# Kernel tuning notes

Measured on AMD Instinct MI355X. Metric: run time of the kernel, lower is better.

## Reference

```python
import jax, jax.numpy as jnp
import numpy as np

N, E, D, G = 20000, 640000, 256, 64
BN_EPS = 1e-5


def setup_inputs() -> dict:
    key = jax.random.key(0)
    ks = jax.random.split(key, 16)
    p = lambda k, sh: jax.random.normal(k, sh, dtype=jnp.float32) * 0.05
    x = jax.random.normal(ks[0], (N, D), dtype=jnp.float32)
    edge_index = jax.random.randint(ks[1], (2, E), 0, N, dtype=jnp.int32)
    batch = jnp.sort(jax.random.randint(ks[2], (N,), 0, G, dtype=jnp.int32))
    return dict(
        x=x, edge_index=edge_index, batch=batch,
        W1=p(ks[3], (D, D)), a1_src=p(ks[4], (D,)), a1_dst=p(ks[5], (D,)), b1=p(ks[6], (D,)),
        W2=p(ks[7], (D, D)), a2_src=p(ks[8], (D,)), a2_dst=p(ks[9], (D,)), b2=p(ks[10], (D,)),
        bn_gamma=jnp.ones((D,), jnp.float32), bn_beta=jnp.zeros((D,), jnp.float32),
        bn_mean=jnp.zeros((D,), jnp.float32), bn_var=jnp.ones((D,), jnp.float32),
        Wl=p(ks[11], (D, D)), bl=p(ks[12], (D,)),
    )


def gat_conv(x, src, dst, W, a_src, a_dst, b):
    # PyG GATConv, heads=1, concat=True, negative_slope=0.2, self-loops already appended
    h = x @ W                               # [N, D]
    alpha_s = h @ a_src                     # [N]
    alpha_d = h @ a_dst                     # [N]
    e = jax.nn.leaky_relu(alpha_s[src] + alpha_d[dst], 0.2)   # [E+N]
    # segment softmax over edges grouped by destination node
    m = jax.ops.segment_max(e, dst, num_segments=N)
    ex = jnp.exp(e - m[dst])
    s = jax.ops.segment_sum(ex, dst, num_segments=N)
    alpha = ex / s[dst]                     # self-loops guarantee s > 0
    out = jax.ops.segment_sum(alpha[:, None] * h[src], dst, num_segments=N)
    return out + b


def reference(x, edge_index, batch, W1, a1_src, a1_dst, b1, W2, a2_src, a2_dst, b2,
              bn_gamma, bn_beta, bn_mean, bn_var, Wl, bl):
    loop = jnp.arange(N, dtype=edge_index.dtype)
    src = jnp.concatenate([edge_index[0], loop])
    dst = jnp.concatenate([edge_index[1], loop])

    h = jax.nn.leaky_relu(gat_conv(x, src, dst, W1, a1_src, a1_dst, b1), 0.01)
    h = jax.nn.leaky_relu(gat_conv(h, src, dst, W2, a2_src, a2_dst, b2), 0.01)
    # BatchNorm over nodes (eval mode, running stats)
    h = (h - bn_mean) * jax.lax.rsqrt(bn_var + BN_EPS) * bn_gamma + bn_beta
    # global mean pool per graph, then linear (dropout is identity in eval)
    sums = jax.ops.segment_sum(h, batch, num_segments=G)           # [G, D]
    cnt = jax.ops.segment_sum(jnp.ones((N,), h.dtype), batch, num_segments=G)
    pooled = sums / jnp.maximum(cnt, 1.0)[:, None]
    return pooled @ Wl.T + bl
```

## Files before the change

kernel.cpp:

```cpp
#include <hip/hip_runtime.h>
#include <hip/hip_bf16.h>

#define NN 20000
#define EE 640000
#define DD 256
#define GG 64
#define ETOT (EE + NN)
#define BN_EPS 1e-5f

#define NPART 8
#define PBLK  128
#define CE    (EE / PBLK)
#define PRNG  (NN / NPART)

#define GBM 64
#define GBN 128
#define GBK 64
#define NGEMMB 626
#define SCE 1023

typedef short s16x8 __attribute__((ext_vector_type(8)));
typedef float f32x4 __attribute__((ext_vector_type(4)));
typedef int   i32x2 __attribute__((ext_vector_type(2)));
typedef int   i32x4 __attribute__((ext_vector_type(4)));

__device__ __forceinline__ unsigned short f2bf_hi(float x) {
    unsigned u = __float_as_uint(x);
    unsigned r = (u + 0x7FFFu + ((u >> 16) & 1u)) >> 16;
    return (unsigned short)r;
}
__device__ __forceinline__ float bf2f(unsigned short h) {
    return __uint_as_float(((unsigned)h) << 16);
}

__device__ __forceinline__ void fma8(const short* __restrict__ hb, int row, int f0,
                                     float a, float* acc) {
    i32x4 hv = *(const i32x4*)(hb + (size_t)row * DD + f0);
    #pragma unroll
    for (int k = 0; k < 4; ++k) {
        unsigned u = (unsigned)hv[k];
        acc[2 * k]     += a * __uint_as_float(u << 16);
        acc[2 * k + 1] += a * __uint_as_float(u & 0xFFFF0000u);
    }
}

__global__ __launch_bounds__(256) void prep_hist_conv_kernel(
        const int* __restrict__ batch, int* __restrict__ start, float* __restrict__ cntf,
        const int* __restrict__ ei, int* __restrict__ counts,
        const float* __restrict__ W1, const float* __restrict__ W2,
        short* __restrict__ BhT1, short* __restrict__ BlT1,
        short* __restrict__ BhT2, short* __restrict__ BlT2) {
    int b = blockIdx.x;
    int r = b & 15, G = b >> 4;
    if (r < 8) {
        int lo = (b & 7) * PRNG;
        int e0 = G * CE;
        for (int i = e0 + threadIdx.x; i < e0 + CE; i += 256) {
            int d = ei[EE + i];
            if ((unsigned)(d - lo) < (unsigned)PRNG) atomicAdd(&counts[d], 1);
        }
        return;
    }
    int idx = G * 8 + (r - 8);
    if (idx < 512) {
        int n = idx & 255, which = idx >> 8;
        int k = threadIdx.x;
        const float* B = which ? W2 : W1;
        short* Bh = which ? BhT2 : BhT1;
        short* Bl = which ? BlT2 : BlT1;
        float x = B[k * DD + n];
        unsigned short hbv = f2bf_hi(x);
        Bh[n * DD + k] = (short)hbv;
        Bl[n * DD + k] = (short)f2bf_hi(x - bf2f(hbv));
    } else if (idx == 512) {
        int g = threadIdx.x;
        if (g <= GG) {
            if (g == GG) start[GG] = NN;
            else {
                int lo = 0, hi = NN;
                while (lo < hi) { int mid = (lo + hi) >> 1; if (batch[mid] < g) lo = mid + 1; else hi = mid; }
                start[g] = lo;
            }
        }
        __syncthreads();
        if (g < GG) cntf[g] = (float)(start[g + 1] - start[g]);
    }
}

#define SCHUNK 20
__global__ __launch_bounds__(1024) void scan_kernel(const int* __restrict__ counts,
                                                    int* __restrict__ offsets,
                                                    int* __restrict__ cursor) {
    __shared__ int wsums[16];
    int t = threadIdx.x, lane = t & 63, wid = t >> 6;
    int base = t * SCHUNK;
    int loc[SCHUNK];
    int sum = 0;
    #pragma unroll
    for (int i = 0; i < SCHUNK; ++i) {
        int idx = base + i;
        int v = (idx < NN) ? (counts[idx] + 1) : 0;
        loc[i] = sum; sum += v;
    }
    int x = sum;
    #pragma unroll
    for (int o = 1; o < 64; o <<= 1) { int tv = __shfl_up(x, o, 64); if (lane >= o) x += tv; }
    if (lane == 63) wsums[wid] = x;
    __syncthreads();
    if (wid == 0) {
        int wv = (lane < 16) ? wsums[lane] : 0;
        #pragma unroll
        for (int o = 1; o < 16; o <<= 1) { int tv = __shfl_up(wv, o, 64); if (lane >= o) wv += tv; }
        if (lane < 16) wsums[lane] = wv;
    }
    __syncthreads();
    int tbase = (wid ? wsums[wid - 1] : 0) + x - sum;
    #pragma unroll
    for (int i = 0; i < SCHUNK; ++i) {
        int idx = base + i;
        if (idx < NN) { int e = tbase + loc[i]; offsets[idx] = e; cursor[idx] = e; }
    }
    if (t == 0) offsets[NN] = wsums[15];
}

template<bool SCAT>
__global__ __launch_bounds__(256) void gemm_kernel(
        const float* __restrict__ A,
        const short* __restrict__ BhT, const short* __restrict__ BlT,
        const float* __restrict__ a_src, const float* __restrict__ a_dst,
        short* __restrict__ hb, float* __restrict__ asp, float* __restrict__ adp, int M,
        const int* __restrict__ ei, int* __restrict__ cursor, int* __restrict__ csr_src) {
    __shared__ short As_h[GBM * GBK];
    __shared__ short As_l[GBM * GBK];
    __shared__ short Bs_h[GBN * GBK];
    __shared__ short Bs_l[GBN * GBK];
    int tid = threadIdx.x;
    int gx = blockIdx.x, gy = blockIdx.y;
    int row0 = gy * GBM;
    int col0 = gx * GBN;
    int w = tid >> 6, lane = tid & 63;
    int wr = w >> 1, wc = w & 1;

    f32x4 acc[2][4];
    #pragma unroll
    for (int m = 0; m < 2; ++m)
        #pragma unroll
        for (int n = 0; n < 4; ++n)
            acc[m][n] = (f32x4){0.f, 0.f, 0.f, 0.f};

    int srow = tid >> 3;
    int sslot = tid & 7;

    for (int k0 = 0; k0 < DD; k0 += GBK) {
        __syncthreads();
        #pragma unroll
        for (int p = 0; p < 2; ++p) {
            int r = p * 32 + srow;
            int gr = row0 + r;
            float xv[8];
            if (gr < M) {
                const float4* ap = (const float4*)(A + (size_t)gr * DD + k0 + sslot * 8);
                float4 a0 = ap[0], a1 = ap[1];
                xv[0] = a0.x; xv[1] = a0.y; xv[2] = a0.z; xv[3] = a0.w;
                xv[4] = a1.x; xv[5] = a1.y; xv[6] = a1.z; xv[7] = a1.w;
            } else {
                #pragma unroll
                for (int i = 0; i < 8; ++i) xv[i] = 0.f;
            }
            s16x8 hv, lv;
            #pragma unroll
            for (int i = 0; i < 8; ++i) {
                unsigned short hbb = f2bf_hi(xv[i]);
                hv[i] = (short)hbb;
                lv[i] = (short)f2bf_hi(xv[i] - bf2f(hbb));
            }
            int byte = r * 128 + ((sslot ^ (r & 7)) << 4);
            *(s16x8*)((char*)As_h + byte) = hv;
            *(s16x8*)((char*)As_l + byte) = lv;
        }
        #pragma unroll
        for (int p = 0; p < 4; ++p) {
            int r = p * 32 + srow;
            int byte = r * 128 + ((sslot ^ (r & 7)) << 4);
            const short* bhp = BhT + (size_t)(col0 + r) * DD + k0 + sslot * 8;
            const short* blp = BlT + (size_t)(col0 + r) * DD + k0 + sslot * 8;
            *(s16x8*)((char*)Bs_h + byte) = *(const s16x8*)bhp;
            *(s16x8*)((char*)Bs_l + byte) = *(const s16x8*)blp;
        }
        __syncthreads();

        #pragma unroll
        for (int ks = 0; ks < 2; ++ks) {
            s16x8 ah[2], al[2], bh[4], bl[4];
            int g = ks * 4 + (lane >> 4);
            #pragma unroll
            for (int m = 0; m < 2; ++m) {
                int r = wr * 32 + m * 16 + (lane & 15);
                int byte = r * 128 + ((g ^ (r & 7)) << 4);
                ah[m] = *(const s16x8*)((char*)As_h + byte);
                al[m] = *(const s16x8*)((char*)As_l + byte);
            }
            #pragma unroll
            for (int n = 0; n < 4; ++n) {
                int c = wc * 64 + n * 16 + (lane & 15);
                int byte = c * 128 + ((g ^ (c & 7)) << 4);
                bh[n] = *(const s16x8*)((char*)Bs_h + byte);
                bl[n] = *(const s16x8*)((char*)Bs_l + byte);
            }
            #pragma unroll
            for (int m = 0; m < 2; ++m)
                #pragma unroll
                for (int n = 0; n < 4; ++n) {
                    acc[m][n] = __builtin_amdgcn_mfma_f32_16x16x32_bf16(ah[m], bh[n], acc[m][n], 0, 0, 0);
                    acc[m][n] = __builtin_amdgcn_mfma_f32_16x16x32_bf16(ah[m], bl[n], acc[m][n], 0, 0, 0);
                    acc[m][n] = __builtin_amdgcn_mfma_f32_16x16x32_bf16(al[m], bh[n], acc[m][n], 0, 0, 0);
                }
        }
    }

    float vsrc[4], vdst[4];
    #pragma unroll
    for (int n = 0; n < 4; ++n) {
        int cg = col0 + wc * 64 + n * 16 + (lane & 15);
        vsrc[n] = a_src[cg];
        vdst[n] = a_dst[cg];
    }
    #pragma unroll
    for (int m = 0; m < 2; ++m) {
        #pragma unroll
        for (int j = 0; j < 4; ++j) {
            float ps = 0.f, pd = 0.f;
            #pragma unroll
            for (int n = 0; n < 4; ++n) {
                float c = acc[m][n][j];
                ps += c * vsrc[n];
                pd += c * vdst[n];
            }
            #pragma unroll
            for (int o = 1; o < 16; o <<= 1) {
                ps += __shfl_xor(ps, o, 64);
                pd += __shfl_xor(pd, o, 64);
            }
            if ((lane & 15) == 0) {
                int rg = row0 + wr * 32 + m * 16 + ((lane >> 4) << 2) + j;
                if (rg < M) {
                    asp[(size_t)(gx * 2 + wc) * NN + rg] = ps;
                    adp[(size_t)(gx * 2 + wc) * NN + rg] = pd;
                }
            }
        }
    }

    #pragma unroll
    for (int m = 0; m < 2; ++m) {
        int rbase = row0 + wr * 32 + m * 16 + ((lane >> 4) << 2);
        #pragma unroll
        for (int n = 0; n < 4; ++n) {
            int cg = col0 + wc * 64 + n * 16 + (lane & 15);
            #pragma unroll
            for (int j = 0; j < 4; ++j) {
                int rg = rbase + j;
                if (rg < M) hb[(size_t)rg * DD + cg] = (short)f2bf_hi(acc[m][n][j]);
            }
        }
    }

    if (SCAT) {
        int bid = gy * 2 + gx;
        int e0 = bid * SCE;
        int e1 = min(e0 + SCE, EE);
        for (int i = e0 + tid; i < e1; i += 256) {
            int d = ei[EE + i];
            int pos = atomicAdd(&cursor[d], 1);
            csr_src[pos] = ei[i];
        }
    }
}

__global__ void reduce_kernel(const float* __restrict__ asp, const float* __restrict__ adp,
                              const int* __restrict__ offsets,
                              float* __restrict__ as_, float* __restrict__ ad_,
                              int* __restrict__ csr_src) {
    int i = blockIdx.x * blockDim.x + threadIdx.x;
    if (i < NN) {
        as_[i] = asp[i] + asp[NN + i] + asp[2 * NN + i] + asp[3 * NN + i];
        ad_[i] = adp[i] + adp[NN + i] + adp[2 * NN + i] + adp[3 * NN + i];
        csr_src[offsets[i + 1] - 1] = i;
    }
}

__global__ __launch_bounds__(256) void alpha_kernel(const int* __restrict__ csr_src,
                                                    const int* __restrict__ offsets,
                                                    const float* __restrict__ as_,
                                                    const float* __restrict__ ad_,
                                                    int2* __restrict__ pairs) {
    int tid = threadIdx.x;
    int w = tid >> 6, lane = tid & 63;
    int node = blockIdx.x * 4 + w;
    int off = offsets[node];
    int deg = offsets[node + 1] - off;
    float adn = ad_[node];

    if (deg <= 64) {
        int si = 0; float e = -INFINITY;
        if (lane < deg) {
            si = csr_src[off + lane];
            float t = as_[si] + adn;
            e = (t > 0.f) ? t : 0.2f * t;
        }
        float m = e;
        #pragma unroll
        for (int o = 32; o > 0; o >>= 1) m = fmaxf(m, __shfl_xor(m, o, 64));
        float ex = (lane < deg) ? expf(e - m) : 0.f;
        float s = ex;
        #pragma unroll
        for (int o = 32; o > 0; o >>= 1) s += __shfl_xor(s, o, 64);
        if (lane < deg) {
            int2 p; p.x = si; p.y = __float_as_int(ex / s);
            pairs[off + lane] = p;
        }
        return;
    }

    float m = -INFINITY, s = 0.f;
    for (int cs = 0; cs < deg; cs += 64) {
        int cl = min(64, deg - cs);
        float e = -INFINITY;
        if (lane < cl) {
            int si = csr_src[off + cs + lane];
            float t = as_[si] + adn;
            e = (t > 0.f) ? t : 0.2f * t;
        }
        float cm = e;
        #pragma unroll
        for (int o = 32; o > 0; o >>= 1) cm = fmaxf(cm, __shfl_xor(cm, o, 64));
        float newm = fmaxf(m, cm);
        float ex = (lane < cl) ? expf(e - newm) : 0.f;
        float csum = ex;
        #pragma unroll
        for (int o = 32; o > 0; o >>= 1) csum += __shfl_xor(csum, o, 64);
        s = s * expf(m - newm) + csum;
        m = newm;
    }
    float inv = 1.f / s;
    for (int cs = 0; cs < deg; cs += 64) {
        int cl = min(64, deg - cs);
        if (lane < cl) {
            int si = csr_src[off + cs + lane];
            float t = as_[si] + adn;
            float e = (t > 0.f) ? t : 0.2f * t;
            int2 p; p.x = si; p.y = __float_as_int(expf(e - m) * inv);
            pairs[off + cs + lane] = p;
        }
    }
}

__global__ __launch_bounds__(256) void aggregate_kernel(const short* __restrict__ hb,
                                                        const int2* __restrict__ pairs,
                                                        const int* __restrict__ offsets,
                                                        const float* __restrict__ bias,
                                                        float* __restrict__ out) {
    int tid = threadIdx.x;
    int w = tid >> 6, lane = tid & 63;
    int b = blockIdx.x;
    int sl = b & 3;
    int node = ((b >> 2) << 2) + w;
    int eg = lane >> 3;
    int fl = lane & 7;
    int f0 = sl * 64 + fl * 8;
    int off = offsets[node];
    int deg = offsets[node + 1] - off;
    const i32x2* pp = (const i32x2*)pairs + off;

    float accA[8], accB[8];
    #pragma unroll
    for (int k = 0; k < 8; ++k) { accA[k] = 0.f; accB[k] = 0.f; }

    int j = 0;
    i32x2 qA, qB;
    if (deg >= 16) { qA = pp[eg]; qB = pp[8 + eg]; }
    for (; j + 32 <= deg; j += 16) {
        i32x2 nA = pp[j + 16 + eg];
        i32x2 nB = pp[j + 24 + eg];
        fma8(hb, qA.x, f0, __int_as_float(qA.y), accA);
        fma8(hb, qB.x, f0, __int_as_float(qB.y), accB);
        qA = nA; qB = nB;
    }
    if (j + 16 <= deg) {
        fma8(hb, qA.x, f0, __int_as_float(qA.y), accA);
        fma8(hb, qB.x, f0, __int_as_float(qB.y), accB);
        j += 16;
    }
    {
        if (j + eg < deg) {
            i32x2 p = pp[j + eg];
            fma8(hb, p.x, f0, __int_as_float(p.y), accA);
        }
        if (j + 8 + eg < deg) {
            i32x2 p = pp[j + 8 + eg];
            fma8(hb, p.x, f0, __int_as_float(p.y), accB);
        }
    }

    f32x4 r0, r1;
    #pragma unroll
    for (int k = 0; k < 8; ++k) {
        float v = accA[k] + accB[k];
        v += __shfl_xor(v, 8, 64);
        v += __shfl_xor(v, 16, 64);
        v += __shfl_xor(v, 32, 64);
        if (k < 4) r0[k] = v; else r1[k - 4] = v;
    }
    if (eg == 0) {
        const f32x4 b0 = *(const f32x4*)(bias + f0);
        const f32x4 b1 = *(const f32x4*)(bias + f0 + 4);
        #pragma unroll
        for (int k = 0; k < 4; ++k) {
            float v0 = r0[k] + b0[k];
            float v1 = r1[k] + b1[k];
            r0[k] = (v0 > 0.f) ? v0 : 0.01f * v0;
            r1[k] = (v1 > 0.f) ? v1 : 0.01f * v1;
        }
        __builtin_nontemporal_store(r0, (f32x4*)(out + (size_t)node * DD + f0));
        __builtin_nontemporal_store(r1, (f32x4*)(out + (size_t)node * DD + f0 + 4));
    }
}

#define PSLICE 8
__global__ __launch_bounds__(256) void pool_kernel(const float* __restrict__ h,
                                                   const int* __restrict__ start,
                                                   float* __restrict__ pool) {
    int g = blockIdx.x >> 3, sl = blockIdx.x & (PSLICE - 1);
    int f = threadIdx.x;
    int s0 = start[g], s1 = start[g + 1];
    float acc = 0.f;
    for (int nd = s0 + sl; nd < s1; nd += PSLICE)
        acc += h[(size_t)nd * DD + f];
    if (acc != 0.f || sl == 0) atomicAdd(&pool[g * DD + f], acc);
}

__global__ __launch_bounds__(256) void final_kernel(const float* __restrict__ pool,
                                                    const float* __restrict__ cnt,
                                                    const float* __restrict__ gam,
                                                    const float* __restrict__ bet,
                                                    const float* __restrict__ mean,
                                                    const float* __restrict__ var,
                                                    const float* __restrict__ Wl,
                                                    const float* __restrict__ bl,
                                                    float* __restrict__ out) {
    __shared__ float p_sh[DD];
    int g = blockIdx.x, j = threadIdx.x;
    float cn = cnt[g];
    float scale = gam[j] * rsqrtf(var[j] + BN_EPS);
    p_sh[j] = (cn > 0.f) ? (pool[g * DD + j] / cn - mean[j]) * scale + bet[j] : 0.f;
    __syncthreads();
    float acc = 0.f;
    for (int fi = 0; fi < DD; ++fi)
        acc += p_sh[fi] * Wl[j * DD + fi];
    out[g * DD + j] = acc + bl[j];
}

extern "C" void kernel_launch(void* const* d_in, const int* in_sizes, int n_in,
                              void* d_out, int out_size, void* d_ws, size_t ws_size,
                              hipStream_t stream) {
    const float* x       = (const float*)d_in[0];
    const int*   ei      = (const int*)d_in[1];
    const int*   batch   = (const int*)d_in[2];
    const float* W1      = (const float*)d_in[3];
    const float* a1_src  = (const float*)d_in[4];
    const float* a1_dst  = (const float*)d_in[5];
    const float* b1      = (const float*)d_in[6];
    const float* W2      = (const float*)d_in[7];
    const float* a2_src  = (const float*)d_in[8];
    const float* a2_dst  = (const float*)d_in[9];
    const float* b2      = (const float*)d_in[10];
    const float* bn_g    = (const float*)d_in[11];
    const float* bn_b    = (const float*)d_in[12];
    const float* bn_m    = (const float*)d_in[13];
    const float* bn_v    = (const float*)d_in[14];
    const float* Wl      = (const float*)d_in[15];
    const float* bl      = (const float*)d_in[16];
    float* out = (float*)d_out;

    char* ws = (char*)d_ws;
    size_t o = 0;
    auto take = [&](size_t bytes) { char* p = ws + o; o += (bytes + 255) & ~(size_t)255; return p; };
    int*   counts  = (int*)  take(NN * 4);
    int*   offsets = (int*)  take((NN + 1) * 4);
    int*   cursor  = (int*)  take(NN * 4);
    int*   csr_src = (int*)  take((size_t)ETOT * 4);
    int2*  pairs   = (int2*) take((size_t)ETOT * 8);
    float* asp     = (float*)take((size_t)4 * NN * 4);
    float* adp     = (float*)take((size_t)4 * NN * 4);
    float* as_     = (float*)take(NN * 4);
    float* ad_     = (float*)take(NN * 4);
    short* hb      = (short*)take((size_t)NN * DD * 2);
    float* bufB    = (float*)take((size_t)NN * DD * 4);
    float* pool    = (float*)take(GG * DD * 4);
    float* cnt     = (float*)take(GG * 4);
    int*   start   = (int*)  take((GG + 1) * 4);
    short* BhT1    = (short*)take((size_t)DD * DD * 2);
    short* BlT1    = (short*)take((size_t)DD * DD * 2);
    short* BhT2    = (short*)take((size_t)DD * DD * 2);
    short* BlT2    = (short*)take((size_t)DD * DD * 2);
    (void)ws_size; (void)in_sizes; (void)n_in; (void)out_size;

    hipMemsetAsync(counts, 0, NN * 4, stream);
    hipMemsetAsync(pool, 0, GG * DD * 4, stream);

    prep_hist_conv_kernel<<<2048, 256, 0, stream>>>(batch, start, cnt, ei, counts,
                                                    W1, W2, BhT1, BlT1, BhT2, BlT2);
    scan_kernel<<<1, 1024, 0, stream>>>(counts, offsets, cursor);

    dim3 ggrid(DD / GBN, (NN + GBM - 1) / GBM);

    gemm_kernel<true><<<ggrid, 256, 0, stream>>>(x, BhT1, BlT1, a1_src, a1_dst,
                                                 hb, asp, adp, NN, ei, cursor, csr_src);
    reduce_kernel<<<(NN + 255) / 256, 256, 0, stream>>>(asp, adp, offsets, as_, ad_, csr_src);
    alpha_kernel<<<NN / 4, 256, 0, stream>>>(csr_src, offsets, as_, ad_, pairs);
    aggregate_kernel<<<NN, 256, 0, stream>>>(hb, pairs, offsets, b1, bufB);

    gemm_kernel<false><<<ggrid, 256, 0, stream>>>(bufB, BhT2, BlT2, a2_src, a2_dst,
                                                  hb, asp, adp, NN, nullptr, nullptr, nullptr);
    reduce_kernel<<<(NN + 255) / 256, 256, 0, stream>>>(asp, adp, offsets, as_, ad_, csr_src);
    alpha_kernel<<<NN / 4, 256, 0, stream>>>(csr_src, offsets, as_, ad_, pairs);
    aggregate_kernel<<<NN, 256, 0, stream>>>(hb, pairs, offsets, b2, bufB);

    pool_kernel<<<GG * PSLICE, 256, 0, stream>>>(bufB, start, pool);
    final_kernel<<<GG, 256, 0, stream>>>(pool, cnt, bn_g, bn_b, bn_m, bn_v, Wl, bl, out);
}
```

Baseline: 275.0 us.

## Partition CSR scatter by destination range and pre-shift source indices to byte offsets

The CSR fill inside the first GEMM now has each block scan a larger edge chunk and keep only edges whose destination falls in one of 8 node ranges. Atomics and csr_src writes from a block therefore land in a narrower, more L2-local region, at the cost of each edge index being read 8 times. Separately, the alpha kernel stores source indices pre-multiplied by the row byte stride (si<<9). This lets the aggregate kernel address hb rows with a plain byte offset instead of a 64-bit multiply per gather. The GEMM grid is also flattened to 1D.

```diff
diff --git a/kernel.cpp b/kernel.cpp
--- a/kernel.cpp
+++ b/kernel.cpp
@@ -17,7 +17,8 @@
 #define GBN 128
 #define GBK 64
 #define NGEMMB 626
-#define SCE 1023
+#define SCHUNKS 78
+#define SCSZ 8206
 
 typedef short s16x8 __attribute__((ext_vector_type(8)));
 typedef float f32x4 __attribute__((ext_vector_type(4)));
@@ -33,9 +34,9 @@
     return __uint_as_float(((unsigned)h) << 16);
 }
 
-__device__ __forceinline__ void fma8(const short* __restrict__ hb, int row, int f0,
-                                     float a, float* acc) {
-    i32x4 hv = *(const i32x4*)(hb + (size_t)row * DD + f0);
+__device__ __forceinline__ void fma8o(const char* __restrict__ hbF, int boff,
+                                      float a, float* acc) {
+    i32x4 hv = *(const i32x4*)(hbF + boff);
     #pragma unroll
     for (int k = 0; k < 4; ++k) {
         unsigned u = (unsigned)hv[k];
@@ -135,7 +136,8 @@
     __shared__ short Bs_h[GBN * GBK];
     __shared__ short Bs_l[GBN * GBK];
     int tid = threadIdx.x;
-    int gx = blockIdx.x, gy = blockIdx.y;
+    int lid = blockIdx.x;
+    int gx = lid & 1, gy = lid >> 1;
     int row0 = gy * GBM;
     int col0 = gx * GBN;
     int w = tid >> 6, lane = tid & 63;
@@ -265,14 +267,17 @@
         }
     }
 
-    if (SCAT) {
-        int bid = gy * 2 + gx;
-        int e0 = bid * SCE;
-        int e1 = min(e0 + SCE, EE);
+    if (SCAT && lid < SCHUNKS * NPART) {
+        int part = lid & 7;
+        int lo = part * PRNG;
+        int e0 = (lid >> 3) * SCSZ;
+        int e1 = min(e0 + SCSZ, EE);
         for (int i = e0 + tid; i < e1; i += 256) {
             int d = ei[EE + i];
-            int pos = atomicAdd(&cursor[d], 1);
-            csr_src[pos] = ei[i];
+            if ((unsigned)(d - lo) < (unsigned)PRNG) {
+                int pos = atomicAdd(&cursor[d], 1);
+                csr_src[pos] = ei[i];
+            }
         }
     }
 }
@@ -316,7 +321,7 @@
         #pragma unroll
         for (int o = 32; o > 0; o >>= 1) s += __shfl_xor(s, o, 64);
         if (lane < deg) {
-            int2 p; p.x = si; p.y = __float_as_int(ex / s);
+            int2 p; p.x = si << 9; p.y = __float_as_int(ex / s);
             pairs[off + lane] = p;
         }
         return;
@@ -349,7 +354,7 @@
             int si = csr_src[off + cs + lane];
             float t = as_[si] + adn;
             float e = (t > 0.f) ? t : 0.2f * t;
-            int2 p; p.x = si; p.y = __float_as_int(expf(e - m) * inv);
+            int2 p; p.x = si << 9; p.y = __float_as_int(expf(e - m) * inv);
             pairs[off + cs + lane] = p;
         }
     }
@@ -368,6 +373,7 @@
     int eg = lane >> 3;
     int fl = lane & 7;
     int f0 = sl * 64 + fl * 8;
+    const char* hbF = (const char*)hb + f0 * 2;
     int off = offsets[node];
     int deg = offsets[node + 1] - off;
     const i32x2* pp = (const i32x2*)pairs + off;
@@ -382,23 +388,23 @@
     for (; j + 32 <= deg; j += 16) {
         i32x2 nA = pp[j + 16 + eg];
         i32x2 nB = pp[j + 24 + eg];
-        fma8(hb, qA.x, f0, __int_as_float(qA.y), accA);
-        fma8(hb, qB.x, f0, __int_as_float(qB.y), accB);
+        fma8o(hbF, qA.x, __int_as_float(qA.y), accA);
+        fma8o(hbF, qB.x, __int_as_float(qB.y), accB);
         qA = nA; qB = nB;
     }
     if (j + 16 <= deg) {
-        fma8(hb, qA.x, f0, __int_as_float(qA.y), accA);
-        fma8(hb, qB.x, f0, __int_as_float(qB.y), accB);
+        fma8o(hbF, qA.x, __int_as_float(qA.y), accA);
+        fma8o(hbF, qB.x, __int_as_float(qB.y), accB);
         j += 16;
     }
     {
         if (j + eg < deg) {
             i32x2 p = pp[j + eg];
-            fma8(hb, p.x, f0, __int_as_float(p.y), accA);
+            fma8o(hbF, p.x, __int_as_float(p.y), accA);
         }
         if (j + 8 + eg < deg) {
             i32x2 p = pp[j + 8 + eg];
-            fma8(hb, p.x, f0, __int_as_float(p.y), accB);
+            fma8o(hbF, p.x, __int_as_float(p.y), accB);
         }
     }
 
@@ -512,16 +518,14 @@
                                                     W1, W2, BhT1, BlT1, BhT2, BlT2);
     scan_kernel<<<1, 1024, 0, stream>>>(counts, offsets, cursor);
 
-    dim3 ggrid(DD / GBN, (NN + GBM - 1) / GBM);
-
-    gemm_kernel<true><<<ggrid, 256, 0, stream>>>(x, BhT1, BlT1, a1_src, a1_dst,
-                                                 hb, asp, adp, NN, ei, cursor, csr_src);
+    gemm_kernel<true><<<NGEMMB, 256, 0, stream>>>(x, BhT1, BlT1, a1_src, a1_dst,
+                                                  hb, asp, adp, NN, ei, cursor, csr_src);
     reduce_kernel<<<(NN + 255) / 256, 256, 0, stream>>>(asp, adp, offsets, as_, ad_, csr_src);
     alpha_kernel<<<NN / 4, 256, 0, stream>>>(csr_src, offsets, as_, ad_, pairs);
     aggregate_kernel<<<NN, 256, 0, stream>>>(hb, pairs, offsets, b1, bufB);
 
-    gemm_kernel<false><<<ggrid, 256, 0, stream>>>(bufB, BhT2, BlT2, a2_src, a2_dst,
-                                                  hb, asp, adp, NN, nullptr, nullptr, nullptr);
+    gemm_kernel<false><<<NGEMMB, 256, 0, stream>>>(bufB, BhT2, BlT2, a2_src, a2_dst,
+                                                   hb, asp, adp, NN, nullptr, nullptr, nullptr);
     reduce_kernel<<<(NN + 255) / 256, 256, 0, stream>>>(asp, adp, offsets, as_, ad_, csr_src);
     alpha_kernel<<<NN / 4, 256, 0, stream>>>(csr_src, offsets, as_, ad_, pairs);
     aggregate_kernel<<<NN, 256, 0, stream>>>(hb, pairs, offsets, b2, bufB);
```

After: 261.8 us. 1.05x faster.
